# Kernel optimization log

Measured on AMD Instinct MI355X. Metric: run time of the kernel, lower is better.

## Reference

```python
import jax, jax.numpy as jnp
import numpy as np

V, E, H, L, B, T = 32000, 512, 512, 2, 64, 256  # vocab, embed, per-layer hidden (1024//2), layers, batch, seq_len


def setup_inputs() -> dict:
    key = jax.random.key(0)
    ks = jax.random.split(key, 8)
    s = 1.0 / np.sqrt(H)  # PyTorch LSTM/Linear uniform init bound
    u = lambda k, shape: jax.random.uniform(k, shape, minval=-s, maxval=s, dtype=jnp.float32)
    return {
        "x": jax.random.randint(ks[0], (B, T), 0, V),
        "embedding": jax.random.normal(ks[1], (V, E), dtype=jnp.float32) * 0.02,
        "W_ih": u(ks[2], (L, 4 * H, E)),   # layer0 input=E, layer1 input=H (E==H here)
        "W_hh": u(ks[3], (L, 4 * H, H)),
        "b_ih": u(ks[4], (L, 4 * H)),
        "b_hh": u(ks[5], (L, 4 * H)),
        "W_fc": u(ks[6], (V, H)),
        "b_fc": u(ks[7], (V,)),
    }


def _lstm_stack(h, c, inp, W_ih, W_hh, b_ih, b_hh):
    # h, c: [L, B, H]; inp: [B, E]. PyTorch gate order: i, f, g, o.
    hs, cs = [], []
    for l in range(W_ih.shape[0]):
        gates = inp @ W_ih[l].T + b_ih[l] + h[l] @ W_hh[l].T + b_hh[l]  # [B, 4H]
        i, f, g, o = jnp.split(gates, 4, axis=-1)
        cn = jax.nn.sigmoid(f) * c[l] + jax.nn.sigmoid(i) * jnp.tanh(g)
        hn = jax.nn.sigmoid(o) * jnp.tanh(cn)
        hs.append(hn)
        cs.append(cn)
        inp = hn
    return jnp.stack(hs), jnp.stack(cs), inp


def reference(x, embedding, W_ih, W_hh, b_ih, b_hh, W_fc, b_fc):
    Bx, Tx = x.shape
    Hd = W_hh.shape[-1]
    Ly = W_ih.shape[0]
    Vx = embedding.shape[0]
    h0 = jnp.zeros((Ly, Bx, Hd), embedding.dtype)
    c0 = jnp.zeros((Ly, Bx, Hd), embedding.dtype)
    x0 = embedding[x[:, 0]]

    def step(carry, _):
        h, c, xt, _ = carry
        h, c, out = _lstm_stack(h, c, xt, W_ih, W_hh, b_ih, b_hh)
        logits = out @ W_fc.T + b_fc                      # [B, V]
        idx = jnp.argmax(logits, axis=1)                   # greedy decode
        xn = embedding[idx]                                # re-embed prediction
        return (h, c, xn, logits), None

    init = (h0, c0, x0, jnp.zeros((Bx, Vx), embedding.dtype))
    (h, c, xn, logits), _ = jax.lax.scan(step, init, None, length=Tx)
    return logits  # logits from the final decode step, [B, V]
```

## Files before the change

kernel.cpp:

```cpp
#include <hip/hip_runtime.h>
#include <stdint.h>

typedef unsigned long long u64;

#define Bq 64
#define Tq 256
#define Hq 512
#define Eq 512
#define Vq 32000

__device__ __forceinline__ float sigmoid_f(float x) { return 1.0f / (1.0f + expf(-x)); }

__device__ __forceinline__ unsigned f2sortable(float f) {
    unsigned u = __float_as_uint(f);
    return (u & 0x80000000u) ? ~u : (u | 0x80000000u);
}

__device__ __forceinline__ void gl_lds16(const float* g, float* l) {
    __builtin_amdgcn_global_load_lds(
        (const __attribute__((address_space(1))) void*)g,
        (__attribute__((address_space(3))) void*)l, 16, 0, 0);
}


#define DOT4(acc, a, wv) \
    acc = fmaf((a).w, (wv).w, fmaf((a).z, (wv).z, fmaf((a).y, (wv).y, fmaf((a).x, (wv).x, (acc)))))

__global__ __launch_bounds__(256) void lstm_layer_kernel(
    const float* __restrict__ emb,
    const int*   __restrict__ xcol,
    const u64*   __restrict__ amax_in,
    const float* __restrict__ inpT,
    const float* __restrict__ hprevT,
    float*       __restrict__ houtT,
    float*       __restrict__ cstate,
    const float* __restrict__ Wih,
    const float* __restrict__ Whh,
    const float* __restrict__ bih,
    const float* __restrict__ bhh,
    u64*         __restrict__ amax_reset,
    int t, int is_layer0)
{
    __shared__ float4 wlds[1024];
    const int h    = blockIdx.x;
    const int tid  = threadIdx.x;
    const int wave = __builtin_amdgcn_readfirstlane(tid >> 6);
    const int lane = tid & 63;

    if (amax_reset && blockIdx.x == 0 && wave == 3) amax_reset[lane] = 0;

    const float4* Wih4 = (const float4*)Wih;
    const float4* Whh4 = (const float4*)Whh;
    #pragma unroll
    for (int i = 0; i < 4; ++i) {
        int g   = i * 256 + tid;
        int s   = g >> 7;
        int off = g & 127;
        const float4* src = (s < 4) ? Wih4 : Whh4;
        wlds[g] = src[(size_t)((s & 3) * Hq + h) * 128 + off];
    }
    __syncthreads();

    const int part = wave >> 1;
    const int kq0  = (wave & 1) << 6;

    float acc0 = 0.f, acc1 = 0.f, acc2 = 0.f, acc3 = 0.f;

    if (part == 0 && is_layer0) {
        int row = (t == 0) ? xcol[lane * Tq] : (int)(~(unsigned)amax_in[lane]);
        const float4* a4 = (const float4*)(emb + (size_t)row * Eq);
        #pragma unroll 4
        for (int i = 0; i < 64; ++i) {
            float4 a = a4[kq0 + i];
            int kq = kq0 + i;
            float4 w0 = wlds[0 * 128 + kq];
            float4 w1 = wlds[1 * 128 + kq];
            float4 w2 = wlds[2 * 128 + kq];
            float4 w3 = wlds[3 * 128 + kq];
            DOT4(acc0, a, w0); DOT4(acc1, a, w1);
            DOT4(acc2, a, w2); DOT4(acc3, a, w3);
        }
    } else {
        const float4* a4 = (const float4*)(part ? hprevT : inpT);
        #pragma unroll 4
        for (int i = 0; i < 64; ++i) {
            int kq = kq0 + i;
            float4 a = a4[kq * 64 + lane];
            float4 w0 = wlds[(part * 4 + 0) * 128 + kq];
            float4 w1 = wlds[(part * 4 + 1) * 128 + kq];
            float4 w2 = wlds[(part * 4 + 2) * 128 + kq];
            float4 w3 = wlds[(part * 4 + 3) * 128 + kq];
            DOT4(acc0, a, w0); DOT4(acc1, a, w1);
            DOT4(acc2, a, w2); DOT4(acc3, a, w3);
        }
    }

    __shared__ float red[4][4][64];
    red[wave][0][lane] = acc0;
    red[wave][1][lane] = acc1;
    red[wave][2][lane] = acc2;
    red[wave][3][lane] = acc3;
    __syncthreads();

    if (wave == 0) {
        float gi = red[0][0][lane] + red[1][0][lane] + red[2][0][lane] + red[3][0][lane]
                 + bih[0 * Hq + h] + bhh[0 * Hq + h];
        float gf = red[0][1][lane] + red[1][1][lane] + red[2][1][lane] + red[3][1][lane]
                 + bih[1 * Hq + h] + bhh[1 * Hq + h];
        float gg = red[0][2][lane] + red[1][2][lane] + red[2][2][lane] + red[3][2][lane]
                 + bih[2 * Hq + h] + bhh[2 * Hq + h];
        float go = red[0][3][lane] + red[1][3][lane] + red[2][3][lane] + red[3][3][lane]
                 + bih[3 * Hq + h] + bhh[3 * Hq + h];
        float cold = cstate[h * 64 + lane];
        float cn = sigmoid_f(gf) * cold + sigmoid_f(gi) * tanhf(gg);
        float hn = sigmoid_f(go) * tanhf(cn);
        cstate[h * 64 + lane] = cn;
        houtT[(h >> 2) * 256 + lane * 4 + (h & 3)] = hn;
    }
}

__global__ __launch_bounds__(256) void fc_kernel(
    const float* __restrict__ hT,
    const float* __restrict__ Wfc,
    const float* __restrict__ bfc,
    float*       __restrict__ out,
    u64*         __restrict__ amax,
    int write_out)
{
    __shared__ float lds[2][8192];
    const int tid  = threadIdx.x;
    const int wave = __builtin_amdgcn_readfirstlane(tid >> 6);
    const int lane = tid & 63;
    const int rgrp = lane >> 3;
    const int bgrp = lane & 7;
    const int v0   = blockIdx.x * 64;

    float acc[8][8];
    #pragma unroll
    for (int j = 0; j < 8; ++j)
        #pragma unroll
        for (int i = 0; i < 8; ++i) acc[j][i] = 0.f;

#define STAGE_CHUNK(cc, dst)                                                  \
    {                                                                         \
        const int k0_ = (cc) * 64;                                            \
        _Pragma("unroll")                                                     \
        for (int it = 0; it < 4; ++it) {                                      \
            int g = it * 256 + tid;                                           \
            int r = g >> 4, sp = g & 15;                                      \
            int gk = k0_ + (((sp ^ (r >> 3)) & 15) << 2);                     \
            gl_lds16(Wfc + (size_t)(v0 + r) * 512 + gk,                       \
                     (dst) + it * 1024 + wave * 256);                         \
        }                                                                     \
        _Pragma("unroll")                                                     \
        for (int it = 0; it < 4; ++it) {                                      \
            int g = it * 256 + tid;                                           \
            int kqr = g >> 6, u = g & 63;                                     \
            int b = (u & 56) | ((u & 7) ^ (u >> 3));                          \
            gl_lds16(hT + (size_t)((cc) * 16 + kqr) * 256 + b * 4,            \
                     (dst) + 4096 + it * 1024 + wave * 256);                  \
        }                                                                     \
    }

    float* cur = lds[0];
    float* nxt = lds[1];

    STAGE_CHUNK(0, cur)
    __syncthreads();

    for (int c = 0; c < 8; ++c) {
        if (c < 7) STAGE_CHUNK(c + 1, nxt)

        #pragma unroll
        for (int kq = 0; kq < 4; ++kq) {
            const int sl = wave * 4 + kq;
            float4 wv[8], av[8];
            #pragma unroll
            for (int j = 0; j < 8; ++j)
                wv[j] = *(const float4*)(cur + (rgrp * 8 + j) * 64 + (((sl ^ rgrp) & 15) << 2));
            #pragma unroll
            for (int i = 0; i < 8; ++i)
                av[i] = *(const float4*)(cur + 4096 + sl * 256 + ((bgrp * 8 + (i ^ bgrp)) << 2));
            #pragma unroll
            for (int j = 0; j < 8; ++j)
                #pragma unroll
                for (int i = 0; i < 8; ++i)
                    DOT4(acc[j][i], av[i], wv[j]);
        }

        __syncthreads();
        float* tmp = cur; cur = nxt; nxt = tmp;
    }

    float* accbuf = lds[0];
    for (int w = 0; w < 4; ++w) {
        if (wave == w) {
            #pragma unroll
            for (int j = 0; j < 8; ++j) {
                float* p = accbuf + (rgrp * 8 + j) * 64 + bgrp * 8;
                if (w == 0) {
                    *(float4*)p       = make_float4(acc[j][0], acc[j][1], acc[j][2], acc[j][3]);
                    *(float4*)(p + 4) = make_float4(acc[j][4], acc[j][5], acc[j][6], acc[j][7]);
                } else {
                    float4 a0 = *(const float4*)p;
                    float4 a1 = *(const float4*)(p + 4);
                    a0.x += acc[j][0]; a0.y += acc[j][1]; a0.z += acc[j][2]; a0.w += acc[j][3];
                    a1.x += acc[j][4]; a1.y += acc[j][5]; a1.z += acc[j][6]; a1.w += acc[j][7];
                    *(float4*)p       = a0;
                    *(float4*)(p + 4) = a1;
                }
            }
        }
        __syncthreads();
    }

    const int b  = tid & 63;
    const int rq = wave;
    float best = -__builtin_huge_valf();
    int bi = 0;
    float lg[16];
    #pragma unroll
    for (int n = 0; n < 16; ++n) {
        int r = rq * 16 + n;
        float v = accbuf[r * 64 + b] + bfc[v0 + r];
        lg[n] = v;
        if (v > best) { best = v; bi = v0 + r; }
    }
    u64 pack = ((u64)f2sortable(best) << 32) | (u64)(~(unsigned)bi);

    u64* redm = (u64*)lds[1];
    redm[rq * 64 + b] = pack;
    __syncthreads();
    if (rq == 0) {
        u64 m  = redm[b];
        u64 m1 = redm[64 + b];  if (m1 > m) m = m1;
        u64 m2 = redm[128 + b]; if (m2 > m) m = m2;
        u64 m3 = redm[192 + b]; if (m3 > m) m = m3;
        atomicMax(&amax[b], m);
    }

    if (write_out) {
        #pragma unroll
        for (int n = 0; n < 16; ++n)
            out[(size_t)b * Vq + v0 + rq * 16 + n] = lg[n];
    }
}

extern "C" void kernel_launch(void* const* d_in, const int* in_sizes, int n_in,
                              void* d_out, int out_size, void* d_ws, size_t ws_size,
                              hipStream_t stream)
{
    const int*   x   = (const int*)d_in[0];
    const float* emb = (const float*)d_in[1];
    const float* Wih = (const float*)d_in[2];
    const float* Whh = (const float*)d_in[3];
    const float* bih = (const float*)d_in[4];
    const float* bhh = (const float*)d_in[5];
    const float* Wfc = (const float*)d_in[6];
    const float* bfc = (const float*)d_in[7];
    float* out = (float*)d_out;

    float* ws = (float*)d_ws;
    float* h0T[2] = { ws,          ws + 32768 };
    float* h1T[2] = { ws + 65536,  ws + 98304 };
    float* c0 = ws + 131072;
    float* c1 = ws + 163840;
    u64* amax = (u64*)(ws + 196608);

    hipMemsetAsync(d_ws, 0, 196608 * sizeof(float) + 64 * sizeof(u64), stream);

    const size_t WL = (size_t)4 * Hq * 512;
    for (int t = 0; t < Tq; ++t) {
        int rd = t & 1, wr = (t + 1) & 1;
        lstm_layer_kernel<<<512, 256, 0, stream>>>(
            emb, x, amax, nullptr, h0T[rd], h0T[wr], c0,
            Wih, Whh, bih, bhh,
            nullptr, t, 1);
        lstm_layer_kernel<<<512, 256, 0, stream>>>(
            emb, x, amax, h0T[wr], h1T[rd], h1T[wr], c1,
            Wih + WL, Whh + WL, bih + 4 * Hq, bhh + 4 * Hq,
            amax, t, 0);
        fc_kernel<<<500, 256, 0, stream>>>(
            h1T[wr], Wfc, bfc, out, amax, (t == Tq - 1) ? 1 : 0);
    }
}
```

Before: 21.18 ms.

## Fuse per-step launches into one persistent kernel with grid barriers

Replaces the 768 separate kernel launches (two LSTM layers plus FC per timestep) with a single persistent kernel of 256 blocks. Each block handles two hidden units or two vocab tiles per phase, and phases are separated by a hierarchical atomic grid barrier. This removes per-launch overhead and the gaps between dependent kernels. In exchange, parallelism per phase is halved, the block must re-stage LSTM weights into LDS on every step, and correctness depends on all 256 blocks being co-resident. The barrier counter is reset at the end of the kernel.

Result: slower. 26.38 ms (+24.6%).

```diff
diff --git a/kernel.cpp b/kernel.cpp
--- a/kernel.cpp
+++ b/kernel.cpp
@@ -26,7 +26,30 @@
 #define DOT4(acc, a, wv) \
     acc = fmaf((a).w, (wv).w, fmaf((a).z, (wv).z, fmaf((a).y, (wv).y, fmaf((a).x, (wv).x, (acc)))))
 
-__global__ __launch_bounds__(256) void lstm_layer_kernel(
+__device__ __attribute__((aligned(64))) unsigned g_bar[160];
+
+__device__ __forceinline__ void gbar(int k) {
+    __syncthreads();
+    if (threadIdx.x == 0) {
+        __threadfence();
+        unsigned* leaf = g_bar + ((blockIdx.x & 7) << 4);
+        unsigned* root = g_bar + 128;
+        unsigned a = __hip_atomic_fetch_add(leaf, 1u, __ATOMIC_ACQ_REL,
+                                            __HIP_MEMORY_SCOPE_AGENT);
+        if (a == (unsigned)(k * 32 + 31))
+            __hip_atomic_fetch_add(root, 1u, __ATOMIC_ACQ_REL,
+                                   __HIP_MEMORY_SCOPE_AGENT);
+        const unsigned tgt = (unsigned)(k * 8 + 8);
+        while (__hip_atomic_load(root, __ATOMIC_RELAXED,
+                                 __HIP_MEMORY_SCOPE_AGENT) < tgt)
+            __builtin_amdgcn_s_sleep(1);
+        __threadfence();
+    }
+    __syncthreads();
+}
+
+__device__ __forceinline__ void lstm_phase(
+    float* smem, int h,
     const float* __restrict__ emb,
     const int*   __restrict__ xcol,
     const u64*   __restrict__ amax_in,
@@ -38,16 +61,14 @@
     const float* __restrict__ Whh,
     const float* __restrict__ bih,
     const float* __restrict__ bhh,
-    u64*         __restrict__ amax_reset,
     int t, int is_layer0)
 {
-    __shared__ float4 wlds[1024];
-    const int h    = blockIdx.x;
+    float4* wlds = (float4*)smem;
+    float (*red)[4][64] = (float (*)[4][64])(smem + 4096);
+
     const int tid  = threadIdx.x;
     const int wave = __builtin_amdgcn_readfirstlane(tid >> 6);
     const int lane = tid & 63;
-
-    if (amax_reset && blockIdx.x == 0 && wave == 3) amax_reset[lane] = 0;
 
     const float4* Wih4 = (const float4*)Wih;
     const float4* Whh4 = (const float4*)Whh;
@@ -67,7 +88,14 @@
     float acc0 = 0.f, acc1 = 0.f, acc2 = 0.f, acc3 = 0.f;
 
     if (part == 0 && is_layer0) {
-        int row = (t == 0) ? xcol[lane * Tq] : (int)(~(unsigned)amax_in[lane]);
+        int row;
+        if (t == 0) {
+            row = xcol[lane * Tq];
+        } else {
+            u64 a = __hip_atomic_load(&amax_in[lane], __ATOMIC_RELAXED,
+                                      __HIP_MEMORY_SCOPE_AGENT);
+            row = (int)(~(unsigned)a);
+        }
         const float4* a4 = (const float4*)(emb + (size_t)row * Eq);
         #pragma unroll 4
         for (int i = 0; i < 64; ++i) {
@@ -95,7 +123,6 @@
         }
     }
 
-    __shared__ float red[4][4][64];
     red[wave][0][lane] = acc0;
     red[wave][1][lane] = acc1;
     red[wave][2][lane] = acc2;
@@ -119,21 +146,46 @@
     }
 }
 
-__global__ __launch_bounds__(256) void fc_kernel(
+__device__ __forceinline__ void fc_stage_chunk(
+    const float* __restrict__ Wfc, const float* __restrict__ hT,
+    int v0, int cc, float* dst, int tid, int wave)
+{
+    const int k0_ = cc * 64;
+    #pragma unroll
+    for (int it = 0; it < 4; ++it) {
+        int g = it * 256 + tid;
+        int r = g >> 4, sp = g & 15;
+        int gk = k0_ + (((sp ^ (r >> 3)) & 15) << 2);
+        gl_lds16(Wfc + (size_t)(v0 + r) * 512 + gk,
+                 dst + it * 1024 + wave * 256);
+    }
+    #pragma unroll
+    for (int it = 0; it < 4; ++it) {
+        int g = it * 256 + tid;
+        int kqr = g >> 6, u = g & 63;
+        int b = (u & 56) | ((u & 7) ^ (u >> 3));
+        gl_lds16(hT + (size_t)(cc * 16 + kqr) * 256 + b * 4,
+                 dst + 4096 + it * 1024 + wave * 256);
+    }
+}
+
+__device__ __forceinline__ void fc_phase(
+    float* smem,
     const float* __restrict__ hT,
     const float* __restrict__ Wfc,
     const float* __restrict__ bfc,
     float*       __restrict__ out,
     u64*         __restrict__ amax,
-    int write_out)
-{
-    __shared__ float lds[2][8192];
+    int write_out, int tile)
+{
+    float* lds0 = smem;
+    float* lds1 = smem + 8192;
     const int tid  = threadIdx.x;
     const int wave = __builtin_amdgcn_readfirstlane(tid >> 6);
     const int lane = tid & 63;
     const int rgrp = lane >> 3;
     const int bgrp = lane & 7;
-    const int v0   = blockIdx.x * 64;
+    const int v0   = tile * 64;
 
     float acc[8][8];
     #pragma unroll
@@ -141,35 +193,14 @@
         #pragma unroll
         for (int i = 0; i < 8; ++i) acc[j][i] = 0.f;
 
-#define STAGE_CHUNK(cc, dst)                                                  \
-    {                                                                         \
-        const int k0_ = (cc) * 64;                                            \
-        _Pragma("unroll")                                                     \
-        for (int it = 0; it < 4; ++it) {                                      \
-            int g = it * 256 + tid;                                           \
-            int r = g >> 4, sp = g & 15;                                      \
-            int gk = k0_ + (((sp ^ (r >> 3)) & 15) << 2);                     \
-            gl_lds16(Wfc + (size_t)(v0 + r) * 512 + gk,                       \
-                     (dst) + it * 1024 + wave * 256);                         \
-        }                                                                     \
-        _Pragma("unroll")                                                     \
-        for (int it = 0; it < 4; ++it) {                                      \
-            int g = it * 256 + tid;                                           \
-            int kqr = g >> 6, u = g & 63;                                     \
-            int b = (u & 56) | ((u & 7) ^ (u >> 3));                          \
-            gl_lds16(hT + (size_t)((cc) * 16 + kqr) * 256 + b * 4,            \
-                     (dst) + 4096 + it * 1024 + wave * 256);                  \
-        }                                                                     \
-    }
-
-    float* cur = lds[0];
-    float* nxt = lds[1];
-
-    STAGE_CHUNK(0, cur)
+    float* cur = lds0;
+    float* nxt = lds1;
+
+    fc_stage_chunk(Wfc, hT, v0, 0, cur, tid, wave);
     __syncthreads();
 
     for (int c = 0; c < 8; ++c) {
-        if (c < 7) STAGE_CHUNK(c + 1, nxt)
+        if (c < 7) fc_stage_chunk(Wfc, hT, v0, c + 1, nxt, tid, wave);
 
         #pragma unroll
         for (int kq = 0; kq < 4; ++kq) {
@@ -192,7 +223,7 @@
         float* tmp = cur; cur = nxt; nxt = tmp;
     }
 
-    float* accbuf = lds[0];
+    float* accbuf = lds0;
     for (int w = 0; w < 4; ++w) {
         if (wave == w) {
             #pragma unroll
@@ -228,7 +259,7 @@
     }
     u64 pack = ((u64)f2sortable(best) << 32) | (u64)(~(unsigned)bi);
 
-    u64* redm = (u64*)lds[1];
+    u64* redm = (u64*)lds1;
     redm[rq * 64 + b] = pack;
     __syncthreads();
     if (rq == 0) {
@@ -243,6 +274,66 @@
         #pragma unroll
         for (int n = 0; n < 16; ++n)
             out[(size_t)b * Vq + v0 + rq * 16 + n] = lg[n];
+    }
+}
+
+__global__ __launch_bounds__(256, 1) void lstm_persistent(
+    const int*   __restrict__ x,
+    const float* __restrict__ emb,
+    const float* __restrict__ Wih,
+    const float* __restrict__ Whh,
+    const float* __restrict__ bih,
+    const float* __restrict__ bhh,
+    const float* __restrict__ Wfc,
+    const float* __restrict__ bfc,
+    float*       __restrict__ out,
+    float*       __restrict__ ws)
+{
+    __shared__ __align__(16) float smem[16384];
+
+    float* h0T0 = ws;
+    float* h0T1 = ws + 32768;
+    float* h1T0 = ws + 65536;
+    float* h1T1 = ws + 98304;
+    float* c0   = ws + 131072;
+    float* c1   = ws + 163840;
+    u64*   amax = (u64*)(ws + 196608);
+
+    const int bid  = blockIdx.x;
+    const int tid  = threadIdx.x;
+    const int wave = tid >> 6;
+    const int lane = tid & 63;
+    const size_t WL = (size_t)4 * Hq * 512;
+
+    int bk = 0;
+    for (int t = 0; t < Tq; ++t) {
+        float* h0rd = (t & 1) ? h0T1 : h0T0;
+        float* h0wr = (t & 1) ? h0T0 : h0T1;
+        float* h1rd = (t & 1) ? h1T1 : h1T0;
+        float* h1wr = (t & 1) ? h1T0 : h1T1;
+
+        lstm_phase(smem, bid,       emb, x, amax, nullptr, h0rd, h0wr, c0,
+                   Wih, Whh, bih, bhh, t, 1);
+        lstm_phase(smem, bid + 256, emb, x, amax, nullptr, h0rd, h0wr, c0,
+                   Wih, Whh, bih, bhh, t, 1);
+        gbar(bk++);
+
+        if (bid == 0 && wave == 3) atomicExch(&amax[lane], 0ull);
+        lstm_phase(smem, bid,       emb, x, amax, h0wr, h1rd, h1wr, c1,
+                   Wih + WL, Whh + WL, bih + 4 * Hq, bhh + 4 * Hq, t, 0);
+        lstm_phase(smem, bid + 256, emb, x, amax, h0wr, h1rd, h1wr, c1,
+                   Wih + WL, Whh + WL, bih + 4 * Hq, bhh + 4 * Hq, t, 0);
+        gbar(bk++);
+
+        fc_phase(smem, h1wr, Wfc, bfc, out, amax, (t == Tq - 1) ? 1 : 0, bid);
+        if (bid + 256 < 500)
+            fc_phase(smem, h1wr, Wfc, bfc, out, amax, (t == Tq - 1) ? 1 : 0, bid + 256);
+        gbar(bk++);
+    }
+
+    if (bid == 0 && tid < 9) {
+        unsigned* p = (tid < 8) ? (g_bar + (tid << 4)) : (g_bar + 128);
+        __hip_atomic_store(p, 0u, __ATOMIC_RELAXED, __HIP_MEMORY_SCOPE_AGENT);
     }
 }
 
@@ -259,28 +350,10 @@
     const float* Wfc = (const float*)d_in[6];
     const float* bfc = (const float*)d_in[7];
     float* out = (float*)d_out;
-
-    float* ws = (float*)d_ws;
-    float* h0T[2] = { ws,          ws + 32768 };
-    float* h1T[2] = { ws + 65536,  ws + 98304 };
-    float* c0 = ws + 131072;
-    float* c1 = ws + 163840;
-    u64* amax = (u64*)(ws + 196608);
+    float* ws  = (float*)d_ws;
 
     hipMemsetAsync(d_ws, 0, 196608 * sizeof(float) + 64 * sizeof(u64), stream);
 
-    const size_t WL = (size_t)4 * Hq * 512;
-    for (int t = 0; t < Tq; ++t) {
-        int rd = t & 1, wr = (t + 1) & 1;
-        lstm_layer_kernel<<<512, 256, 0, stream>>>(
-            emb, x, amax, nullptr, h0T[rd], h0T[wr], c0,
-            Wih, Whh, bih, bhh,
-            nullptr, t, 1);
-        lstm_layer_kernel<<<512, 256, 0, stream>>>(
-            emb, x, amax, h0T[wr], h1T[rd], h1T[wr], c1,
-            Wih + WL, Whh + WL, bih + 4 * Hq, bhh + 4 * Hq,
-            amax, t, 0);
-        fc_kernel<<<500, 256, 0, stream>>>(
-            h1T[wr], Wfc, bfc, out, amax, (t == Tq - 1) ? 1 : 0);
-    }
-}
+    lstm_persistent<<<dim3(256), dim3(256), 0, stream>>>(
+        x, emb, Wih, Whh, bih, bhh, Wfc, bfc, out, ws);
+}
```

## Convert FC weights to fp16 once and stream them in the vocab projection

Applied to the files above, without the earlier changes.

Adds a one-time kernel that converts W_fc to fp16 in workspace, plus an FC kernel that stages the fp16 weights (with a non-temporal load hint) and converts them to fp32 for the FMAs. This halves the weight bytes read on each of the 256 decode steps, which is the main memory traffic. The fp16 rounding can change argmax picks in the greedy loop and so change the final logits. The new path runs only when the workspace is large enough.

New measurement: 22.15 ms. 4.6% more time.

```diff
diff --git a/kernel.cpp b/kernel.cpp
--- a/kernel.cpp
+++ b/kernel.cpp
@@ -2,6 +2,7 @@
 #include <stdint.h>
 
 typedef unsigned long long u64;
+typedef _Float16 h4 __attribute__((ext_vector_type(4)));
 
 #define Bq 64
 #define Tq 256
@@ -22,9 +23,32 @@
         (__attribute__((address_space(3))) void*)l, 16, 0, 0);
 }
 
+__device__ __forceinline__ void gl_lds16_nt(const void* g, float* l) {
+    __builtin_amdgcn_global_load_lds(
+        (const __attribute__((address_space(1))) void*)g,
+        (__attribute__((address_space(3))) void*)l, 16, 0, 2);
+}
+
 
 #define DOT4(acc, a, wv) \
     acc = fmaf((a).w, (wv).w, fmaf((a).z, (wv).z, fmaf((a).y, (wv).y, fmaf((a).x, (wv).x, (acc)))))
+
+#define DOT4H(acc, a, wv) \
+    acc = fmaf((a).w, (float)(wv).w, fmaf((a).z, (float)(wv).z, \
+          fmaf((a).y, (float)(wv).y, fmaf((a).x, (float)(wv).x, (acc)))))
+
+__global__ __launch_bounds__(256) void wfc_to_f16(
+    const float4* __restrict__ w4, uint4* __restrict__ o4)
+{
+    size_t i = (size_t)blockIdx.x * 256 + threadIdx.x;
+    float4 a = w4[2 * i], b = w4[2 * i + 1];
+    union { _Float16 h[8]; uint4 u; } p;
+    p.h[0] = (_Float16)a.x; p.h[1] = (_Float16)a.y;
+    p.h[2] = (_Float16)a.z; p.h[3] = (_Float16)a.w;
+    p.h[4] = (_Float16)b.x; p.h[5] = (_Float16)b.y;
+    p.h[6] = (_Float16)b.z; p.h[7] = (_Float16)b.w;
+    o4[i] = p.u;
+}
 
 __global__ __launch_bounds__(256) void lstm_layer_kernel(
     const float* __restrict__ emb,
@@ -119,6 +143,136 @@
     }
 }
 
+__global__ __launch_bounds__(256) void fc_kernel_f16(
+    const float*    __restrict__ hT,
+    const _Float16* __restrict__ Wh,
+    const float*    __restrict__ bfc,
+    float*          __restrict__ out,
+    u64*            __restrict__ amax,
+    int write_out)
+{
+    __shared__ float lds[2][6144];
+    const int tid  = threadIdx.x;
+    const int wave = __builtin_amdgcn_readfirstlane(tid >> 6);
+    const int lane = tid & 63;
+    const int rgrp = lane >> 3;
+    const int bgrp = lane & 7;
+    const int v0   = blockIdx.x * 64;
+
+    float acc[8][8];
+    #pragma unroll
+    for (int j = 0; j < 8; ++j)
+        #pragma unroll
+        for (int i = 0; i < 8; ++i) acc[j][i] = 0.f;
+
+#define STAGE16(cc, dst)                                                      \
+    {                                                                         \
+        _Pragma("unroll")                                                     \
+        for (int it = 0; it < 2; ++it) {                      \
+            int g = it * 256 + tid;                                           \
+            int r = g >> 3, s = g & 7;                                        \
+            gl_lds16_nt(Wh + (size_t)(v0 + r) * 512 + (cc) * 64              \
+                           + (((s ^ (r >> 3)) & 7) << 3),                     \
+                        (dst) + it * 1024 + wave * 256);                      \
+        }                                                                     \
+        _Pragma("unroll")                                                     \
+        for (int it = 0; it < 4; ++it) {                 \
+            int g = it * 256 + tid;                                           \
+            int kqr = g >> 6, u = g & 63;                                     \
+            int b = (u & 56) | ((u & 7) ^ (u >> 3));                          \
+            gl_lds16(hT + (size_t)((cc) * 16 + kqr) * 256 + b * 4,            \
+                     (dst) + 2048 + it * 1024 + wave * 256);                  \
+        }                                                                     \
+    }
+
+    float* cur = lds[0];
+    float* nxt = lds[1];
+
+    STAGE16(0, cur)
+    __syncthreads();
+
+    for (int c = 0; c < 8; ++c) {
+        if (c < 7) STAGE16(c + 1, nxt)
+
+        #pragma unroll
+        for (int kq = 0; kq < 4; ++kq) {
+            const int sl = wave * 4 + kq;
+            const _Float16* wbase = (const _Float16*)cur;
+            h4 wv[8];
+            float4 av[8];
+            #pragma unroll
+            for (int j = 0; j < 8; ++j)
+                wv[j] = *(const h4*)(wbase + (rgrp * 8 + j) * 64
+                                     + ((((sl >> 1) ^ rgrp) & 7) << 3)
+                                     + ((sl & 1) << 2));
+            #pragma unroll
+            for (int i = 0; i < 8; ++i)
+                av[i] = *(const float4*)(cur + 2048 + sl * 256 + ((bgrp * 8 + (i ^ bgrp)) << 2));
+            #pragma unroll
+            for (int j = 0; j < 8; ++j)
+                #pragma unroll
+                for (int i = 0; i < 8; ++i)
+                    DOT4H(acc[j][i], av[i], wv[j]);
+        }
+
+        __syncthreads();
+        float* tmp = cur; cur = nxt; nxt = tmp;
+    }
+
+    float* accbuf = lds[0];
+    for (int w = 0; w < 4; ++w) {
+        if (wave == w) {
+            #pragma unroll
+            for (int j = 0; j < 8; ++j) {
+                float* p = accbuf + (rgrp * 8 + j) * 64 + bgrp * 8;
+                if (w == 0) {
+                    *(float4*)p       = make_float4(acc[j][0], acc[j][1], acc[j][2], acc[j][3]);
+                    *(float4*)(p + 4) = make_float4(acc[j][4], acc[j][5], acc[j][6], acc[j][7]);
+                } else {
+                    float4 a0 = *(const float4*)p;
+                    float4 a1 = *(const float4*)(p + 4);
+                    a0.x += acc[j][0]; a0.y += acc[j][1]; a0.z += acc[j][2]; a0.w += acc[j][3];
+                    a1.x += acc[j][4]; a1.y += acc[j][5]; a1.z += acc[j][6]; a1.w += acc[j][7];
+                    *(float4*)p       = a0;
+                    *(float4*)(p + 4) = a1;
+                }
+            }
+        }
+        __syncthreads();
+    }
+
+    const int b  = tid & 63;
+    const int rq = wave;
+    float best = -__builtin_huge_valf();
+    int bi = 0;
+    float lg[16];
+    #pragma unroll
+    for (int n = 0; n < 16; ++n) {
+        int r = rq * 16 + n;
+        float v = accbuf[r * 64 + b] + bfc[v0 + r];
+        lg[n] = v;
+        if (v > best) { best = v; bi = v0 + r; }
+    }
+    u64 pack = ((u64)f2sortable(best) << 32) | (u64)(~(unsigned)bi);
+
+    u64* redm = (u64*)lds[1];
+    redm[rq * 64 + b] = pack;
+    __syncthreads();
+    if (rq == 0) {
+        u64 m  = redm[b];
+        u64 m1 = redm[64 + b];  if (m1 > m) m = m1;
+        u64 m2 = redm[128 + b]; if (m2 > m) m = m2;
+        u64 m3 = redm[192 + b]; if (m3 > m) m = m3;
+        atomicMax(&amax[b], m);
+    }
+
+    if (write_out) {
+        #pragma unroll
+        for (int n = 0; n < 16; ++n)
+            out[(size_t)b * Vq + v0 + rq * 16 + n] = lg[n];
+    }
+}
+
 __global__ __launch_bounds__(256) void fc_kernel(
     const float* __restrict__ hT,
     const float* __restrict__ Wfc,
@@ -267,7 +421,15 @@
     float* c1 = ws + 163840;
     u64* amax = (u64*)(ws + 196608);
 
+    const size_t W16_OFF   = 262144;
+    const size_t need_ws   = W16_OFF * 4 + (size_t)Vq * 512 * 2;
+    const int    use_f16   = (ws_size >= need_ws);
+    _Float16*    w16       = (_Float16*)(ws + W16_OFF);
+
     hipMemsetAsync(d_ws, 0, 196608 * sizeof(float) + 64 * sizeof(u64), stream);
+
+    if (use_f16)
+        wfc_to_f16<<<8000, 256, 0, stream>>>((const float4*)Wfc, (uint4*)w16);
 
     const size_t WL = (size_t)4 * Hq * 512;
     for (int t = 0; t < Tq; ++t) {
@@ -280,7 +442,11 @@
             emb, x, amax, h0T[wr], h1T[rd], h1T[wr], c1,
             Wih + WL, Whh + WL, bih + 4 * Hq, bhh + 4 * Hq,
             amax, t, 0);
-        fc_kernel<<<500, 256, 0, stream>>>(
-            h1T[wr], Wfc, bfc, out, amax, (t == Tq - 1) ? 1 : 0);
-    }
-}
+        if (use_f16)
+            fc_kernel_f16<<<500, 256, 0, stream>>>(
+                h1T[wr], w16, bfc, out, amax, (t == Tq - 1) ? 1 : 0);
+        else
+            fc_kernel<<<500, 256, 0, stream>>>(
+                h1T[wr], Wfc, bfc, out, amax, (t == Tq - 1) ? 1 : 0);
+    }
+}
```
